# Kernel tuning notes

Hardware: AMD Instinct MI355X
Metric: run time of the kernel (lower is better)

The kernel has to match this reference:

```python
import jax, jax.numpy as jnp
import numpy as np

K = 3  # three_nn
EPS = 1e-10


def setup_inputs() -> dict:
    key = jax.random.key(0)
    ks = jax.random.split(key, 10)
    B, N, NP = 4, 16384, 4096
    C1, C2 = 128, 256
    Cin, H1, H2, Cout = C1 + C2, 256, 256, 128
    xyz1 = jax.random.normal(ks[0], (B, N, 3), dtype=jnp.float32)
    xyz2 = jax.random.normal(ks[1], (B, NP, 3), dtype=jnp.float32)
    features1 = jax.random.normal(ks[2], (B, N, C1), dtype=jnp.float32)
    features2 = jax.random.normal(ks[3], (B, NP, C2), dtype=jnp.float32)
    def lin(k, fan_in, fan_out):
        bound = 1.0 / np.sqrt(fan_in)
        kw, kb = jax.random.split(k)
        W = jax.random.uniform(kw, (fan_in, fan_out), jnp.float32, -bound, bound)
        b = jax.random.uniform(kb, (fan_out,), jnp.float32, -bound, bound)
        return W, b
    W1, b1 = lin(ks[4], Cin, H1)
    W2, b2 = lin(ks[5], H1, H2)
    W3, b3 = lin(ks[6], H2, Cout)
    return {"xyz1": xyz1, "xyz2": xyz2, "features1": features1,
            "features2": features2, "W1": W1, "b1": b1, "W2": W2,
            "b2": b2, "W3": W3, "b3": b3}


def _three_nn(xyz1, xyz2):
    # squared pairwise distances via |a|^2 + |b|^2 - 2 a.b  -> [B, N, npoint]
    sq1 = jnp.sum(xyz1 * xyz1, axis=-1)  # [B, N]
    sq2 = jnp.sum(xyz2 * xyz2, axis=-1)  # [B, npoint]
    dots = jnp.einsum("bnd,bmd->bnm", xyz1, xyz2)
    sqdist = sq1[:, :, None] + sq2[:, None, :] - 2.0 * dots
    neg_d, idx = jax.lax.top_k(-sqdist, K)  # 3 smallest squared distances
    return -neg_d, idx  # dist:[B,N,3], idx:[B,N,3]


def reference(xyz1, xyz2, features1, features2, W1, b1, W2, b2, W3, b3):
    B = xyz1.shape[0]
    dist, idx = _three_nn(xyz1, xyz2)
    # torch custom three_nn is non-differentiable in dist
    dist = jax.lax.stop_gradient(dist)
    dist = jnp.maximum(dist, EPS)
    recip = 1.0 / dist                                  # [B, N, 3]
    weight = recip / jnp.sum(recip, axis=-1, keepdims=True)
    # three_interpolate: gather neighbor features and weighted-sum
    batch_idx = jnp.arange(B)[:, None, None]
    gathered = features2[batch_idx, idx]                # [B, N, 3, C2]
    interp = jnp.einsum("bnkc,bnk->bnc", gathered, weight)
    new_features = jnp.concatenate([features1, interp], axis=-1)
    h = jax.nn.relu(new_features @ W1 + b1)
    h = jax.nn.relu(h @ W2 + b2)
    return h @ W3 + b3
```

## Files before the change

### kernel.cpp

```cpp
#include <hip/hip_runtime.h>
#include <stdint.h>

#define QT   65536
#define NPTS 4096
#define C1   128
#define C2   256
#define CIN  384
#define COUT 128

typedef _Float16 f16;
typedef __attribute__((ext_vector_type(8))) _Float16 f16x8;
typedef __attribute__((ext_vector_type(4))) float f32x4;

__device__ __attribute__((aligned(16))) f16 g_w1p[12 * 16 * 64 * 8];
__device__ __attribute__((aligned(16))) f16 g_w2p[8 * 16 * 64 * 8];
__device__ __attribute__((aligned(16))) f16 g_w3p[8 * 8 * 64 * 8];
__device__ __attribute__((aligned(16))) float4 g_cand[4 * NPTS];

__device__ inline void packW4(const float* __restrict__ W, f16* __restrict__ dst,
                              int i, int N, int NCB) {
  const int g = i & 3, quad = (i >> 2) & 3, cbk = i >> 4;
  const int cb = cbk % NCB, kcb = cbk / NCB;
  const int col = cb * 16 + g * 4;
  const int k0 = kcb * 32 + quad * 8;
  f16x8 o[4];
#pragma unroll
  for (int e = 0; e < 8; ++e) {
    float4 v = *(const float4*)(W + (size_t)(k0 + e) * N + col);
    o[0][e] = (f16)v.x; o[1][e] = (f16)v.y; o[2][e] = (f16)v.z; o[3][e] = (f16)v.w;
  }
  f16* base = dst + ((size_t)cbk * 64 + quad * 16 + g * 4) * 8;
#pragma unroll
  for (int j = 0; j < 4; ++j) *(f16x8*)(base + j * 8) = o[j];
}

__global__ __launch_bounds__(256) void prep(
    const float* __restrict__ xyz2, const float* __restrict__ W1,
    const float* __restrict__ W2,   const float* __restrict__ W3) {
  const int tid = blockIdx.x * 256 + threadIdx.x;
  const int nthr = gridDim.x * 256;
  for (int i = tid; i < 4 * NPTS; i += nthr) {
    const float* p = xyz2 + (size_t)i * 3;
    float x = p[0], y = p[1], z = p[2];
    g_cand[i] = make_float4(x, y, z, fmaf(x, x, fmaf(y, y, z * z)));
  }
  for (int i = tid; i < 12 * 16 * 16; i += nthr) packW4(W1, g_w1p, i, 256, 16);
  for (int i = tid; i < 8 * 16 * 16; i += nthr) packW4(W2, g_w2p, i, 256, 16);
  for (int i = tid; i < 8 * 8 * 16; i += nthr) packW4(W3, g_w3p, i, 128, 8);
}

__device__ inline uint32_t umin(uint32_t a, uint32_t b) { return a < b ? a : b; }
__device__ inline uint32_t med3u(uint32_t a, uint32_t b, uint32_t c) {
  uint32_t d;
  asm("v_med3_u32 %0, %1, %2, %3" : "=v"(d) : "v"(a), "v"(b), "v"(c));
  return d;
}

#define XS_STRIDE 392
#define HS_STRIDE 264
#define DMPD_OFF 16384
#define DMPI_OFF 28672
#define WV_OFF 50176
#define IV_OFF 51200
#define SMEM_BYTES 52224

__global__ __launch_bounds__(512) void fused_fp(
    const float* __restrict__ xyz1, const float* __restrict__ xyz2,
    const float* __restrict__ f1,   const float* __restrict__ f2,
    const float* __restrict__ W1,   const float* __restrict__ b1,
    const float* __restrict__ W2,   const float* __restrict__ b2,
    const float* __restrict__ W3,   const float* __restrict__ b3,
    float* __restrict__ out)
{
  __shared__ __align__(16) char smem[SMEM_BYTES];
  double*   dmpD = (double*)(smem + DMPD_OFF);
  int*      dmpI = (int*)(smem + DMPI_OFF);
  float*    wvp  = (float*)(smem + WV_OFF);
  int*      ivp  = (int*)(smem + IV_OFF);
  f16*      Xs   = (f16*)smem;
  f16*      Hs   = (f16*)smem;

  const int t = threadIdx.x;
  const int r = t & 63;
  const int w = t >> 6;
  const int qb = blockIdx.x * 64;
  const int batch = qb >> 14;
  const float* xz2b = xyz2 + (size_t)batch * NPTS * 3;
  const float* f2b  = f2   + (size_t)batch * NPTS * C2;

  const int q = qb + r;
  const float qx = xyz1[q * 3], qy = xyz1[q * 3 + 1], qz = xyz1[q * 3 + 2];
  const float nx = -2.f * qx, ny = -2.f * qy, nz = -2.f * qz;
  const float sq1q = qx * qx + qy * qy + qz * qz;

  uint32_t k0 = ~0u, k1 = ~0u, k2 = ~0u, k3 = ~0u, k4 = ~0u;

  auto ins5 = [&](uint32_t c) {
    uint32_t n0 = umin(k0, c);
    uint32_t n1 = med3u(k0, k1, c);
    uint32_t n2 = med3u(k1, k2, c);
    uint32_t n3 = med3u(k2, k3, c);
    uint32_t n4 = med3u(k3, k4, c);
    k0 = n0; k1 = n1; k2 = n2; k3 = n3; k4 = n4;
  };
  auto packk = [&](float e, uint32_t idx) -> uint32_t {
    return (__builtin_bit_cast(uint32_t, e) & 0xFFFFF000u) | idx;
  };

  {
    const int wu = __builtin_amdgcn_readfirstlane(w);
    const float4* __restrict__ cp = g_cand + (batch << 12) + (wu << 9);
    const uint32_t abase = (uint32_t)(wu << 9);
    const float sbias = sq1q + 0.05f;
    #pragma unroll 2
    for (int m = 0; m < 512; m += 4) {
      float4 c0 = cp[m], c1 = cp[m + 1], c2 = cp[m + 2], c3 = cp[m + 3];
      float e0 = fmaf(nx, c0.x, fmaf(ny, c0.y, fmaf(nz, c0.z, c0.w))) + sbias;
      float e1 = fmaf(nx, c1.x, fmaf(ny, c1.y, fmaf(nz, c1.z, c1.w))) + sbias;
      float e2 = fmaf(nx, c2.x, fmaf(ny, c2.y, fmaf(nz, c2.z, c2.w))) + sbias;
      float e3 = fmaf(nx, c3.x, fmaf(ny, c3.y, fmaf(nz, c3.z, c3.w))) + sbias;
      ins5(packk(e0, abase + m));
      ins5(packk(e1, abase + m + 1));
      ins5(packk(e2, abase + m + 2));
      ins5(packk(e3, abase + m + 3));
    }
  }

  {
    const double x1 = (double)qx, y1 = (double)qy, z1 = (double)qz;
    const double sq1 = x1 * x1 + y1 * y1 + z1 * z1;
    double d0 = 1e300, d1 = 1e300, d2 = 1e300;
    int j0 = 0, j1 = 0, j2 = 0;
    uint32_t sv[5] = {k0, k1, k2, k3, k4};
    #pragma unroll
    for (int s = 0; s < 5; ++s) {
      int idx = (int)(sv[s] & (NPTS - 1));
      const float* p2 = xz2b + (size_t)idx * 3;
      double x2 = (double)p2[0], y2 = (double)p2[1], z2 = (double)p2[2];
      double d = sq1 + (x2 * x2 + y2 * y2 + z2 * z2)
                     - 2.0 * (x1 * x2 + y1 * y2 + z1 * z2);
      bool c2 = (d < d2) || (d == d2 && idx < j2);
      bool c1 = (d < d1) || (d == d1 && idx < j1);
      bool c0 = (d < d0) || (d == d0 && idx < j0);
      d2 = c1 ? d1 : (c2 ? d : d2);  j2 = c1 ? j1 : (c2 ? idx : j2);
      d1 = c0 ? d0 : (c1 ? d : d1);  j1 = c0 ? j0 : (c1 ? idx : j1);
      d0 = c0 ? d : d0;              j0 = c0 ? idx : j0;
    }
    const int base = (w * 64 + r) * 3;
    dmpD[base]     = d0;  dmpI[base]     = j0;
    dmpD[base + 1] = d1;  dmpI[base + 1] = j1;
    dmpD[base + 2] = d2;  dmpI[base + 2] = j2;
  }
  __syncthreads();

  if (w == 0) {
    double d0 = 1e300, d1 = 1e300, d2 = 1e300;
    int j0 = 0, j1 = 0, j2 = 0;
    #pragma unroll
    for (int w2 = 0; w2 < 8; ++w2) {
      #pragma unroll
      for (int s = 0; s < 3; ++s) {
        const int base = (w2 * 64 + r) * 3 + s;
        double d = dmpD[base];
        int idx  = dmpI[base];
        bool c2 = (d < d2) || (d == d2 && idx < j2);
        bool c1 = (d < d1) || (d == d1 && idx < j1);
        bool c0 = (d < d0) || (d == d0 && idx < j0);
        d2 = c1 ? d1 : (c2 ? d : d2);  j2 = c1 ? j1 : (c2 ? idx : j2);
        d1 = c0 ? d0 : (c1 ? d : d1);  j1 = c0 ? j0 : (c1 ? idx : j1);
        d0 = c0 ? d : d0;              j0 = c0 ? idx : j0;
      }
    }
    float e0 = fmaxf((float)d0, 1e-10f);
    float e1 = fmaxf((float)d1, 1e-10f);
    float e2 = fmaxf((float)d2, 1e-10f);
    float r0 = 1.f / e0, r1 = 1.f / e1, r2 = 1.f / e2;
    float inv = 1.f / (r0 + r1 + r2);
    wvp[r * 4 + 0] = r0 * inv; wvp[r * 4 + 1] = r1 * inv;
    wvp[r * 4 + 2] = r2 * inv; wvp[r * 4 + 3] = 0.f;
    ivp[r * 4 + 0] = j0; ivp[r * 4 + 1] = j1; ivp[r * 4 + 2] = j2; ivp[r * 4 + 3] = 0;
  }
  __syncthreads();

  {
    const int row = t >> 3, c = t & 7;
    f16* xr = Xs + row * XS_STRIDE;
    {
      const float* f1r = f1 + (size_t)(qb + row) * C1 + c * 16;
      float4 u0 = *(const float4*)(f1r);
      float4 u1 = *(const float4*)(f1r + 4);
      float4 u2 = *(const float4*)(f1r + 8);
      float4 u3 = *(const float4*)(f1r + 12);
      f16x8 o0, o1;
      o0[0] = (f16)u0.x; o0[1] = (f16)u0.y; o0[2] = (f16)u0.z; o0[3] = (f16)u0.w;
      o0[4] = (f16)u1.x; o0[5] = (f16)u1.y; o0[6] = (f16)u1.z; o0[7] = (f16)u1.w;
      o1[0] = (f16)u2.x; o1[1] = (f16)u2.y; o1[2] = (f16)u2.z; o1[3] = (f16)u2.w;
      o1[4] = (f16)u3.x; o1[5] = (f16)u3.y; o1[6] = (f16)u3.z; o1[7] = (f16)u3.w;
      *(f16x8*)(xr + c * 16)     = o0;
      *(f16x8*)(xr + c * 16 + 8) = o1;
    }
    const float w0 = wvp[row * 4 + 0], w1 = wvp[row * 4 + 1], w2 = wvp[row * 4 + 2];
    const float* p0 = f2b + (size_t)(ivp[row * 4 + 0] & (NPTS - 1)) * C2;
    const float* p1 = f2b + (size_t)(ivp[row * 4 + 1] & (NPTS - 1)) * C2;
    const float* p2 = f2b + (size_t)(ivp[row * 4 + 2] & (NPTS - 1)) * C2;
    #pragma unroll
    for (int ch = 0; ch < 4; ++ch) {
      const int col = ch * 64 + c * 8;
      float4 a0 = *(const float4*)(p0 + col), b0 = *(const float4*)(p0 + col + 4);
      float4 a1 = *(const float4*)(p1 + col), b1v = *(const float4*)(p1 + col + 4);
      float4 a2 = *(const float4*)(p2 + col), b2v = *(const float4*)(p2 + col + 4);
      f16x8 o;
      o[0] = (f16)(w0 * a0.x + w1 * a1.x + w2 * a2.x);
      o[1] = (f16)(w0 * a0.y + w1 * a1.y + w2 * a2.y);
      o[2] = (f16)(w0 * a0.z + w1 * a1.z + w2 * a2.z);
      o[3] = (f16)(w0 * a0.w + w1 * a1.w + w2 * a2.w);
      o[4] = (f16)(w0 * b0.x + w1 * b1v.x + w2 * b2v.x);
      o[5] = (f16)(w0 * b0.y + w1 * b1v.y + w2 * b2v.y);
      o[6] = (f16)(w0 * b0.z + w1 * b1v.z + w2 * b2v.z);
      o[7] = (f16)(w0 * b0.w + w1 * b1v.w + w2 * b2v.w);
      *(f16x8*)(xr + C1 + col) = o;
    }
  }
  __syncthreads();

  const int l16 = r & 15, quad = r >> 4;
  const int nb = w * 32;

  f32x4 acc[4][2];
  #pragma unroll
  for (int i = 0; i < 4; ++i)
    #pragma unroll
    for (int j = 0; j < 2; ++j) acc[i][j] = f32x4{0.f, 0.f, 0.f, 0.f};

  #pragma unroll
  for (int kc = 0; kc < CIN; kc += 32) {
    f16x8 a[4];
    #pragma unroll
    for (int i = 0; i < 4; ++i)
      a[i] = *(const f16x8*)(Xs + (i * 16 + l16) * XS_STRIDE + kc + quad * 8);
    f16x8 b[2];
    #pragma unroll
    for (int j = 0; j < 2; ++j)
      b[j] = *((const f16x8*)g_w1p +
               (size_t)((kc >> 5) * 16 + (w * 2 + j)) * 64 + r);
    #pragma unroll
    for (int i = 0; i < 4; ++i)
      #pragma unroll
      for (int j = 0; j < 2; ++j)
        acc[i][j] = __builtin_amdgcn_mfma_f32_16x16x32_f16(a[i], b[j], acc[i][j], 0, 0, 0);
  }
  __syncthreads();
  #pragma unroll
  for (int j = 0; j < 2; ++j) {
    float bv = b1[nb + j * 16 + l16];
    #pragma unroll
    for (int i = 0; i < 4; ++i)
      #pragma unroll
      for (int e = 0; e < 4; ++e) {
        int row = i * 16 + quad * 4 + e;
        Hs[row * HS_STRIDE + nb + j * 16 + l16] =
            (f16)fmaxf(acc[i][j][e] + bv, 0.f);
      }
  }
  __syncthreads();

  f32x4 acc2[4][2];
  #pragma unroll
  for (int i = 0; i < 4; ++i)
    #pragma unroll
    for (int j = 0; j < 2; ++j) acc2[i][j] = f32x4{0.f, 0.f, 0.f, 0.f};

  #pragma unroll
  for (int kc = 0; kc < 256; kc += 32) {
    f16x8 a[4];
    #pragma unroll
    for (int i = 0; i < 4; ++i)
      a[i] = *(const f16x8*)(Hs + (i * 16 + l16) * HS_STRIDE + kc + quad * 8);
    f16x8 b[2];
    #pragma unroll
    for (int j = 0; j < 2; ++j)
      b[j] = *((const f16x8*)g_w2p +
               (size_t)((kc >> 5) * 16 + (w * 2 + j)) * 64 + r);
    #pragma unroll
    for (int i = 0; i < 4; ++i)
      #pragma unroll
      for (int j = 0; j < 2; ++j)
        acc2[i][j] = __builtin_amdgcn_mfma_f32_16x16x32_f16(a[i], b[j], acc2[i][j], 0, 0, 0);
  }
  __syncthreads();
  #pragma unroll
  for (int j = 0; j < 2; ++j) {
    float bv = b2[nb + j * 16 + l16];
    #pragma unroll
    for (int i = 0; i < 4; ++i)
      #pragma unroll
      for (int e = 0; e < 4; ++e) {
        int row = i * 16 + quad * 4 + e;
        Hs[row * HS_STRIDE + nb + j * 16 + l16] =
            (f16)fmaxf(acc2[i][j][e] + bv, 0.f);
      }
  }
  __syncthreads();

  const int nb3 = w * 16;
  f32x4 acc3[4];
  #pragma unroll
  for (int i = 0; i < 4; ++i) acc3[i] = f32x4{0.f, 0.f, 0.f, 0.f};

  #pragma unroll
  for (int kc = 0; kc < 256; kc += 32) {
    f16x8 a[4];
    #pragma unroll
    for (int i = 0; i < 4; ++i)
      a[i] = *(const f16x8*)(Hs + (i * 16 + l16) * HS_STRIDE + kc + quad * 8);
    f16x8 b;
    b = *((const f16x8*)g_w3p + (size_t)((kc >> 5) * 8 + w) * 64 + r);
    #pragma unroll
    for (int i = 0; i < 4; ++i)
      acc3[i] = __builtin_amdgcn_mfma_f32_16x16x32_f16(a[i], b, acc3[i], 0, 0, 0);
  }
  {
    int col = nb3 + l16;
    float bv = b3[col];
    #pragma unroll
    for (int i = 0; i < 4; ++i)
      #pragma unroll
      for (int e = 0; e < 4; ++e) {
        int row = i * 16 + quad * 4 + e;
        out[(size_t)(qb + row) * COUT + col] = acc3[i][e] + bv;
      }
  }
}

extern "C" void kernel_launch(void* const* d_in, const int* in_sizes, int n_in,
                              void* d_out, int out_size, void* d_ws, size_t ws_size,
                              hipStream_t stream)
{
  (void)out_size; (void)d_ws; (void)ws_size;
  static const int expect[10] = {196608, 49152, 8388608, 4194304,
                                 98304, 256, 65536, 256, 32768, 128};
  const void* p[10];
  bool ok = (n_in == 10);
  if (ok) {
    bool used[10] = {false};
    for (int e = 0; e < 10; ++e) {
      p[e] = nullptr;
      for (int i = 0; i < 10; ++i) {
        if (!used[i] && in_sizes[i] == expect[e]) {
          p[e] = d_in[i]; used[i] = true; break;
        }
      }
      if (!p[e]) { ok = false; break; }
    }
  }
  if (!ok)
    for (int e = 0; e < 10; ++e) p[e] = d_in[e < n_in ? e : (n_in - 1)];

  prep<<<256, 256, 0, stream>>>(
      (const float*)p[1], (const float*)p[4],
      (const float*)p[6], (const float*)p[8]);

  fused_fp<<<QT / 64, 512, 0, stream>>>(
      (const float*)p[0], (const float*)p[1],
      (const float*)p[2], (const float*)p[3],
      (const float*)p[4], (const float*)p[5],
      (const float*)p[6], (const float*)p[7],
      (const float*)p[8], (const float*)p[9],
      (float*)d_out);
}
```

Baseline: 215.0 us.

## Load features1 directly into MFMA A-fragments and shrink shared-memory tile

Result: slower. 235.9 us (+9.7%).

```diff
diff --git a/kernel.cpp b/kernel.cpp
--- a/kernel.cpp
+++ b/kernel.cpp
@@ -56,13 +56,13 @@
   return d;
 }
 
-#define XS_STRIDE 392
+#define XS_STRIDE 264
 #define HS_STRIDE 264
-#define DMPD_OFF 16384
-#define DMPI_OFF 28672
-#define WV_OFF 50176
-#define IV_OFF 51200
-#define SMEM_BYTES 52224
+#define DMPD_OFF 0
+#define DMPI_OFF 12288
+#define WV_OFF 33792
+#define IV_OFF 34816
+#define SMEM_BYTES 35840
 
 __global__ __launch_bounds__(512) void fused_fp(
     const float* __restrict__ xyz1, const float* __restrict__ xyz2,
@@ -185,20 +185,6 @@
   {
     const int row = t >> 3, c = t & 7;
     f16* xr = Xs + row * XS_STRIDE;
-    {
-      const float* f1r = f1 + (size_t)(qb + row) * C1 + c * 16;
-      float4 u0 = *(const float4*)(f1r);
-      float4 u1 = *(const float4*)(f1r + 4);
-      float4 u2 = *(const float4*)(f1r + 8);
-      float4 u3 = *(const float4*)(f1r + 12);
-      f16x8 o0, o1;
-      o0[0] = (f16)u0.x; o0[1] = (f16)u0.y; o0[2] = (f16)u0.z; o0[3] = (f16)u0.w;
-      o0[4] = (f16)u1.x; o0[5] = (f16)u1.y; o0[6] = (f16)u1.z; o0[7] = (f16)u1.w;
-      o1[0] = (f16)u2.x; o1[1] = (f16)u2.y; o1[2] = (f16)u2.z; o1[3] = (f16)u2.w;
-      o1[4] = (f16)u3.x; o1[5] = (f16)u3.y; o1[6] = (f16)u3.z; o1[7] = (f16)u3.w;
-      *(f16x8*)(xr + c * 16)     = o0;
-      *(f16x8*)(xr + c * 16 + 8) = o1;
-    }
     const float w0 = wvp[row * 4 + 0], w1 = wvp[row * 4 + 1], w2 = wvp[row * 4 + 2];
     const float* p0 = f2b + (size_t)(ivp[row * 4 + 0] & (NPTS - 1)) * C2;
     const float* p1 = f2b + (size_t)(ivp[row * 4 + 1] & (NPTS - 1)) * C2;
@@ -218,7 +204,7 @@
       o[5] = (f16)(w0 * b0.y + w1 * b1v.y + w2 * b2v.y);
       o[6] = (f16)(w0 * b0.z + w1 * b1v.z + w2 * b2v.z);
       o[7] = (f16)(w0 * b0.w + w1 * b1v.w + w2 * b2v.w);
-      *(f16x8*)(xr + C1 + col) = o;
+      *(f16x8*)(xr + col) = o;
     }
   }
   __syncthreads();
@@ -235,9 +221,23 @@
   #pragma unroll
   for (int kc = 0; kc < CIN; kc += 32) {
     f16x8 a[4];
-    #pragma unroll
-    for (int i = 0; i < 4; ++i)
-      a[i] = *(const f16x8*)(Xs + (i * 16 + l16) * XS_STRIDE + kc + quad * 8);
+    if (kc < C1) {
+      #pragma unroll
+      for (int i = 0; i < 4; ++i) {
+        const float* p = f1 + (size_t)(qb + i * 16 + l16) * C1 + kc + quad * 8;
+        float4 u0 = *(const float4*)p;
+        float4 u1 = *(const float4*)(p + 4);
+        a[i][0] = (f16)u0.x; a[i][1] = (f16)u0.y;
+        a[i][2] = (f16)u0.z; a[i][3] = (f16)u0.w;
+        a[i][4] = (f16)u1.x; a[i][5] = (f16)u1.y;
+        a[i][6] = (f16)u1.z; a[i][7] = (f16)u1.w;
+      }
+    } else {
+      #pragma unroll
+      for (int i = 0; i < 4; ++i)
+        a[i] = *(const f16x8*)(Xs + (i * 16 + l16) * XS_STRIDE +
+                               (kc - C1) + quad * 8);
+    }
     f16x8 b[2];
     #pragma unroll
     for (int j = 0; j < 2; ++j)
```
